# Optimization experiments

Measured on AMD Instinct MI355X. Metric: run time of the kernel, lower is better.

The kernel has to match this reference:

```python
import jax, jax.numpy as jnp
import numpy as np

NEG_SLOPE = 0.2  # LeakyReLU slope used throughout the torch module
K = 20           # hard-coded in Net.__init__ (self.k = 20)


def leaky(x):
    return jnp.where(x >= 0, x, NEG_SLOPE * x)


def setup_inputs() -> dict:
    key = jax.random.key(0)
    ks = jax.random.split(key, 11)
    B, N = 8, 2048
    Cin, Co = 6, 64  # AGConv(3*2, 64, 3*2)
    x = jax.random.normal(ks[0], (B, 3, N), dtype=jnp.float32)
    # 1x1 conv weights (bias=False in the torch code)
    W0 = jax.random.normal(ks[1], (Co, Cin), dtype=jnp.float32) / np.sqrt(Cin)      # AGConv.conv0
    W1 = jax.random.normal(ks[2], (Co * Cin, Co), dtype=jnp.float32) / np.sqrt(Co)  # AGConv.conv1
    Wc = jax.random.normal(ks[3], (3, Co), dtype=jnp.float32) / np.sqrt(Co)         # Net.conv1
    # inference-mode BatchNorm folded to per-channel scale/shift
    bn0_s = jax.random.uniform(ks[4], (Co,), minval=0.5, maxval=1.5)
    bn0_b = 0.1 * jax.random.normal(ks[5], (Co,))
    bn1_s = jax.random.uniform(ks[6], (Co,), minval=0.5, maxval=1.5)
    bn1_b = 0.1 * jax.random.normal(ks[7], (Co,))
    bnc_s = jax.random.uniform(ks[8], (3,), minval=0.5, maxval=1.5)
    bnc_b = 0.1 * jax.random.normal(ks[9], (3,))
    return dict(x=x, W0=W0, bn0_s=bn0_s, bn0_b=bn0_b, W1=W1, bn1_s=bn1_s,
                bn1_b=bn1_b, Wc=Wc, bnc_s=bnc_s, bnc_b=bnc_b)


def reference(x, W0, bn0_s, bn0_b, W1, bn1_s, bn1_b, Wc, bnc_s, bnc_b):
    B, C, N = x.shape  # [B, 3, N]
    xt = jnp.transpose(x, (0, 2, 1))  # [B, N, 3]
    inner = jnp.einsum('bci,bcj->bij', x, x)          # [B, N, N]
    xx = jnp.sum(x * x, axis=1)                       # [B, N]
    pd = 2.0 * inner - xx[:, :, None] - xx[:, None, :]
    _, idx = jax.lax.top_k(pd, K)                     # [B, N, K] int32
    # get_graph_feature: gather neighbor coords, concat (nbr - ctr, ctr)
    nbr = xt[jnp.arange(B)[:, None, None], idx]       # [B, N, K, 3]
    ctr = jnp.broadcast_to(xt[:, :, None, :], (B, N, K, C))
    e = jnp.concatenate([nbr - ctr, ctr], axis=-1)    # [B, N, K, 6]
    # p == e here since both get_graph_feature calls use the same input & idx
    # AGConv: generate per-edge [64,6] weights from e, apply to e
    y = leaky(jnp.einsum('bnki,oi->bnko', e, W0) * bn0_s + bn0_b)   # [B, N, K, 64]
    y = jnp.einsum('bnko,po->bnkp', y, W1).reshape(B, N, K, 64, 6)  # per-edge weight mats
    out = jnp.einsum('bnkoi,bnki->bnko', y, e)                      # adaptive conv
    out = leaky(out * bn1_s + bn1_b)                                # [B, N, K, 64]
    # max-pool aggregate over neighbors
    x1 = jnp.max(out, axis=2)                                       # [B, N, 64]
    # Net.conv1: 1x1 conv 64->3 + BN + leaky
    z = leaky(jnp.einsum('bno,co->bnc', x1, Wc) * bnc_s + bnc_b)    # [B, N, 3]
    return jnp.transpose(z, (0, 2, 1))                              # [B, 3, N]
```

## Files before the change

### kernel.cpp

```cpp
#include <hip/hip_runtime.h>

#define NEGSLOPE 0.2f
#define NINF (-3.4e38f)

typedef _Float16 half8 __attribute__((ext_vector_type(8)));
typedef float f32x4 __attribute__((ext_vector_type(4)));
typedef unsigned long long u64;

#define YSTRIDE 72

__device__ __forceinline__ half8 h8zero() {
    half8 z;
#pragma unroll
    for (int i = 0; i < 8; ++i) z[i] = (_Float16)0.f;
    return z;
}

__device__ __forceinline__ unsigned umin(unsigned a, unsigned b) { return a < b ? a : b; }
__device__ __forceinline__ unsigned umax(unsigned a, unsigned b) { return a > b ? a : b; }

template <int CTRL>
__device__ __forceinline__ unsigned dpp_movm(unsigned v) {
    return (unsigned)__builtin_amdgcn_update_dpp(-1, (int)v, CTRL, 0xF, 0xF, false);
}

__global__ __launch_bounds__(256) void topk_kernel(
    const float* __restrict__ x, int* __restrict__ idx_out,
    const float* __restrict__ w1, _Float16* __restrict__ w1g,
    const float* __restrict__ w0, _Float16* __restrict__ w0f,
    f32x4* __restrict__ xt) {
    if (blockIdx.x >= 4096) {
        const int pid = blockIdx.x - 4096;
        int tid = pid * 256 + threadIdx.x;
#pragma unroll
        for (int it = 0; it < 12; ++it, tid += 2048) {
            int j = tid & 7;
            int L = (tid >> 3) & 63;
            int r = tid >> 9;
            int t4 = r & 3;
            int ks = r >> 2;
            int q = L >> 4, c = L & 15;
            int i = ks >> 1;
            int o = 32 * (ks & 1) + 8 * q + j;
            int u = 16 * t4 + c;
            w1g[tid] = (_Float16)w1[(u * 6 + i) * 64 + o];
        }
        if (pid == 0) {
#pragma unroll
            for (int s = 0; s < 2; ++s) {
                int t2 = threadIdx.x * 2 + s;
                int r8 = t2 >> 3, j = t2 & 7;
                w0f[t2] = (j < 6) ? (_Float16)w0[r8 * 6 + j] : (_Float16)0.f;
            }
        }
        int base = pid * 2048;
#pragma unroll
        for (int it = 0; it < 8; ++it) {
            int i = base + it * 256 + threadIdx.x;
            int bb = i >> 11, n = i & 2047;
            const float* xbp = x + bb * 6144;
            xt[i] = (f32x4){xbp[n], xbp[2048 + n], xbp[4096 + n], 0.f};
        }
        return;
    }

    const int wave = threadIdx.x >> 6;
    const int lane = threadIdx.x & 63;
    const int row = blockIdx.x * 4 + wave;
    const int b = row >> 11;
    const int n = row & 2047;
    const float* xb = x + b * 6144;
    const float xn0 = xb[n];
    const float xn1 = xb[2048 + n];
    const float xn2 = xb[4096 + n];

    unsigned r0 = 0xFFFFFFFFu, r1 = 0xFFFFFFFFu;
    unsigned r2 = 0xFFFFFFFFu, r3 = 0xFFFFFFFFu;
    unsigned g5k = 0xFFFFFFFFu;

#pragma unroll
    for (int t = 0; t < 32; ++t) {
        const int j = t * 64 + lane;
        const float dx = xb[j] - xn0;
        const float dy = xb[2048 + j] - xn1;
        const float dz = xb[4096 + j] - xn2;
        const float d = dx * dx + dy * dy + dz * dz;
        unsigned p = (__float_as_uint(d) & 0xFFFFF800u) | (unsigned)j;
        unsigned q0 = umin(r0, p); p = umax(r0, p); r0 = q0;
        unsigned q1 = umin(r1, p); p = umax(r1, p); r1 = q1;
        unsigned q2 = umin(r2, p); p = umax(r2, p); r2 = q2;
        unsigned q3 = umin(r3, p); p = umax(r3, p); r3 = q3;
        g5k = umin(g5k, p);
    }

    if (lane & 1) {
        unsigned t0 = r0; r0 = r3; r3 = t0;
        unsigned t1 = r1; r1 = r2; r2 = t1;
    }

#define CROSS(DL, KK)                                                         \
    {                                                                         \
        const bool asc = ((lane >> ((KK) - 2)) & 1) == 0;                     \
        const bool low = (lane & (DL)) == 0;                                  \
        const bool selmin = (asc == low);                                     \
        const unsigned p0 = (unsigned)__shfl_xor((int)r0, (DL), 64);          \
        const unsigned p1 = (unsigned)__shfl_xor((int)r1, (DL), 64);          \
        const unsigned p2 = (unsigned)__shfl_xor((int)r2, (DL), 64);          \
        const unsigned p3 = (unsigned)__shfl_xor((int)r3, (DL), 64);          \
        r0 = selmin ? umin(r0, p0) : umax(r0, p0);                            \
        r1 = selmin ? umin(r1, p1) : umax(r1, p1);                            \
        r2 = selmin ? umin(r2, p2) : umax(r2, p2);                            \
        r3 = selmin ? umin(r3, p3) : umax(r3, p3);                            \
    }
#define INLANE(KK)                                                            \
    {                                                                         \
        const bool asc = ((lane >> ((KK) - 2)) & 1) == 0;                     \
        { unsigned lo = umin(r0, r2), hi = umax(r0, r2);                      \
          r0 = asc ? lo : hi; r2 = asc ? hi : lo; }                           \
        { unsigned lo = umin(r1, r3), hi = umax(r1, r3);                      \
          r1 = asc ? lo : hi; r3 = asc ? hi : lo; }                           \
        { unsigned lo = umin(r0, r1), hi = umax(r0, r1);                      \
          r0 = asc ? lo : hi; r1 = asc ? hi : lo; }                           \
        { unsigned lo = umin(r2, r3), hi = umax(r2, r3);                      \
          r2 = asc ? lo : hi; r3 = asc ? hi : lo; }                           \
    }

    CROSS(1, 3)  INLANE(3)
    CROSS(2, 4)  CROSS(1, 4)  INLANE(4)
    CROSS(4, 5)  CROSS(2, 5)  CROSS(1, 5)  INLANE(5)
    CROSS(8, 6)  CROSS(4, 6)  CROSS(2, 6)  CROSS(1, 6)  INLANE(6)
    CROSS(16, 7) CROSS(8, 7)  CROSS(4, 7)  CROSS(2, 7)  CROSS(1, 7)  INLANE(7)
    CROSS(32, 8) CROSS(16, 8) CROSS(8, 8)  CROSS(4, 8)  CROSS(2, 8)  CROSS(1, 8)
    INLANE(8)
#undef CROSS
#undef INLANE

    const int out_base = row * 20;
    const unsigned T20p = (unsigned)__builtin_amdgcn_readlane((int)r3, 4);
    const u64 bad = __ballot(g5k < T20p);

    if (bad == 0) {
        if (lane < 5) {
            int4 v;
            v.x = (int)(r0 & 2047u); v.y = (int)(r1 & 2047u);
            v.z = (int)(r2 & 2047u); v.w = (int)(r3 & 2047u);
            *(int4*)(idx_out + out_base + lane * 4) = v;
        }
    } else {
        unsigned Tprev = 0u;
#pragma unroll 1
        for (int r = 0; r < 20; ++r) {
            unsigned best = 0xFFFFFFFFu;
#pragma unroll
            for (int t = 0; t < 32; ++t) {
                const int j = t * 64 + lane;
                const float dx = xb[j] - xn0;
                const float dy = xb[2048 + j] - xn1;
                const float dz = xb[4096 + j] - xn2;
                const float d = dx * dx + dy * dy + dz * dz;
                const unsigned p = (__float_as_uint(d) & 0xFFFFF800u) | (unsigned)j;
                const bool ok = (r == 0) || (p > Tprev);
                best = umin(best, ok ? p : 0xFFFFFFFFu);
            }
            { unsigned o = dpp_movm<0x111>(best); best = umin(best, o); }
            { unsigned o = dpp_movm<0x112>(best); best = umin(best, o); }
            { unsigned o = dpp_movm<0x114>(best); best = umin(best, o); }
            { unsigned o = dpp_movm<0x118>(best); best = umin(best, o); }
            { unsigned o = dpp_movm<0x142>(best); best = umin(best, o); }
            { unsigned o = dpp_movm<0x143>(best); best = umin(best, o); }
            const unsigned K = (unsigned)__builtin_amdgcn_readlane((int)best, 63);
            if (lane == 0) idx_out[out_base + r] = (int)(K & 2047u);
            Tprev = K;
        }
    }
}

__global__ __launch_bounds__(128, 3) void mlp_mfma(
    const f32x4* __restrict__ xt, const int* __restrict__ idx,
    const _Float16* __restrict__ w0f, const float* __restrict__ bn0s,
    const float* __restrict__ bn0b, const _Float16* __restrict__ w1g,
    const float* __restrict__ bn1s, const float* __restrict__ bn1b,
    const float* __restrict__ wc, const float* __restrict__ bncs,
    const float* __restrict__ bncb, float* __restrict__ out) {
    __shared__ __align__(16) _Float16 yL[2][80 * YSTRIDE];
    __shared__ __align__(16) half8 eL[2][80];
    const int wave = threadIdx.x >> 6;
    const int lane = threadIdx.x & 63;
    const int q = lane >> 4, c = lane & 15;
    const int gw = blockIdx.x * 2 + wave;
    const int b = gw >> 9;
    const int P0 = (gw & 511) * 4;
    _Float16* yw = yL[wave];
    half8* ew = eL[wave];
    const f32x4* xtb = xt + (b << 11);

    {
        const int k = lane >> 2, pt = lane & 3;
        const int n = P0 + pt;
        const int j = idx[(b * 2048 + n) * 20 + k];
        const f32x4 cc = xtb[n];
        const f32x4 nb = xtb[j];
        half8 ev;
        ev[0] = (_Float16)(nb[0] - cc[0]); ev[1] = (_Float16)(nb[1] - cc[1]);
        ev[2] = (_Float16)(nb[2] - cc[2]); ev[3] = (_Float16)cc[0];
        ev[4] = (_Float16)cc[1];           ev[5] = (_Float16)cc[2];
        ev[6] = (_Float16)0.f;             ev[7] = (_Float16)0.f;
        ew[lane] = ev;
    }
    if (lane < 16) {
        const int el = 64 + lane;
        const int k = el >> 2, pt = el & 3;
        const int n = P0 + pt;
        const int j = idx[(b * 2048 + n) * 20 + k];
        const f32x4 cc = xtb[n];
        const f32x4 nb = xtb[j];
        half8 ev;
        ev[0] = (_Float16)(nb[0] - cc[0]); ev[1] = (_Float16)(nb[1] - cc[1]);
        ev[2] = (_Float16)(nb[2] - cc[2]); ev[3] = (_Float16)cc[0];
        ev[4] = (_Float16)cc[1];           ev[5] = (_Float16)cc[2];
        ev[6] = (_Float16)0.f;             ev[7] = (_Float16)0.f;
        ew[el] = ev;
    }

    const half8* w0f8 = (const half8*)w0f;
    const half8 z8 = h8zero();
    half8 B1[4];
    float s0v[4], b0v[4];
#pragma unroll
    for (int nt = 0; nt < 4; ++nt) {
        const half8 v = w0f8[nt * 16 + c];
        B1[nt] = (q == 0) ? v : z8;
        s0v[nt] = bn0s[16 * nt + c];
        b0v[nt] = bn0b[16 * nt + c];
    }
#pragma unroll
    for (int mt = 0; mt < 5; ++mt) {
        const half8 ev = ew[16 * mt + c];
        const half8 Ae = (q == 0) ? ev : z8;
        const int ebase = 16 * mt + 4 * q;
#pragma unroll
        for (int nt = 0; nt < 4; ++nt) {
            f32x4 D = {0.f, 0.f, 0.f, 0.f};
            D = __builtin_amdgcn_mfma_f32_16x16x32_f16(Ae, B1[nt], D, 0, 0, 0);
#pragma unroll
            for (int r = 0; r < 4; ++r) {
                float v = D[r] * s0v[nt] + b0v[nt];
                v = fmaxf(v, NEGSLOPE * v);
                const int edge = ebase + r;
                yw[edge * YSTRIDE + ((16 * nt + c) ^ (edge & 0x38))] =
                    (_Float16)v;
            }
        }
    }

    const half8* w1g8 = (const half8*)w1g;

    f32x4 acc[5][4];
#pragma unroll
    for (int mm = 0; mm < 5; ++mm)
#pragma unroll
        for (int t4 = 0; t4 < 4; ++t4) acc[mm][t4] = (f32x4){0.f, 0.f, 0.f, 0.f};

#pragma unroll 1
    for (int i6 = 0; i6 < 6; ++i6) {
        _Float16 es[5];
#pragma unroll
        for (int mm = 0; mm < 5; ++mm)
            es[mm] = ((const _Float16*)(ew + 16 * mm + c))[i6];
#pragma unroll
        for (int ks2 = 0; ks2 < 2; ++ks2) {
            const int ks = 2 * i6 + ks2;
            half8 B[4];
#pragma unroll
            for (int t4 = 0; t4 < 4; ++t4)
                B[t4] = w1g8[(ks * 4 + t4) * 64 + lane];
#pragma unroll
            for (int mm = 0; mm < 5; ++mm) {
                const int rrow = 16 * mm + c;
                const half8 Af = *(const half8*)&yw[rrow * YSTRIDE +
                                                    ((32 * ks2 + 8 * q) ^ (rrow & 0x38))];
                const half8 An = Af * es[mm];
#pragma unroll
                for (int t4 = 0; t4 < 4; ++t4)
                    acc[mm][t4] = __builtin_amdgcn_mfma_f32_16x16x32_f16(
                        An, B[t4], acc[mm][t4], 0, 0, 0);
            }
        }
    }

    float bs1[4], bb1[4];
#pragma unroll
    for (int t4 = 0; t4 < 4; ++t4) {
        bs1[t4] = bn1s[16 * t4 + c];
        bb1[t4] = bn1b[16 * t4 + c];
    }

    float x1[4][4];
#pragma unroll
    for (int r = 0; r < 4; ++r)
#pragma unroll
        for (int t4 = 0; t4 < 4; ++t4) {
            float v = NINF;
#pragma unroll
            for (int mm = 0; mm < 5; ++mm) {
                float w = acc[mm][t4][r] * bs1[t4] + bb1[t4];
                w = fmaxf(w, NEGSLOPE * w);
                v = fmaxf(v, w);
            }
            v = fmaxf(v, __shfl_xor(v, 16, 64));
            v = fmaxf(v, __shfl_xor(v, 32, 64));
            x1[r][t4] = v;
        }

    float wcv[3][4];
#pragma unroll
    for (int co = 0; co < 3; ++co)
#pragma unroll
        for (int t4 = 0; t4 < 4; ++t4) wcv[co][t4] = wc[co * 64 + 16 * t4 + c];

    float part[4][3];
#pragma unroll
    for (int r = 0; r < 4; ++r)
#pragma unroll
        for (int co = 0; co < 3; ++co) {
            float s = x1[r][0] * wcv[co][0] + x1[r][1] * wcv[co][1] +
                      x1[r][2] * wcv[co][2] + x1[r][3] * wcv[co][3];
#pragma unroll
            for (int d = 1; d < 16; d <<= 1) s += __shfl_xor(s, d, 64);
            part[r][co] = s;
        }

    if (c == 0 && q < 3) {
        const float sc = bncs[q], bc = bncb[q];
#pragma unroll
        for (int r = 0; r < 4; ++r) {
            float z = part[r][q] * sc + bc;
            z = fmaxf(z, NEGSLOPE * z);
            out[(b * 3 + q) * 2048 + P0 + r] = z;
        }
    }
}

extern "C" void kernel_launch(void* const* d_in, const int* in_sizes, int n_in,
                              void* d_out, int out_size, void* d_ws, size_t ws_size,
                              hipStream_t stream) {
    const float* x    = (const float*)d_in[0];
    const float* W0   = (const float*)d_in[1];
    const float* bn0s = (const float*)d_in[2];
    const float* bn0b = (const float*)d_in[3];
    const float* W1   = (const float*)d_in[4];
    const float* bn1s = (const float*)d_in[5];
    const float* bn1b = (const float*)d_in[6];
    const float* Wc   = (const float*)d_in[7];
    const float* bncs = (const float*)d_in[8];
    const float* bncb = (const float*)d_in[9];

    _Float16* w1g = (_Float16*)d_ws;
    _Float16* w0f = (_Float16*)((char*)d_ws + 49152);
    f32x4* xt = (f32x4*)((char*)d_ws + 65536);
    int* idx = (int*)((char*)d_ws + 327680);

    topk_kernel<<<4104, 256, 0, stream>>>(x, idx, W1, w1g, W0, w0f, xt);
    mlp_mfma<<<2048, 128, 0, stream>>>(xt, idx, w0f, bn0s, bn0b, w1g,
                                       bn1s, bn1b, Wc, bncs, bncb,
                                       (float*)d_out);
}
```

Measured before the change: 138.0 us.

## Process two query points per wave and replace bitonic merge with radix threshold search

Each wave now handles two query rows, sharing the coordinate loads for candidate points across both distance computations, and the grid is halved to match. The per-lane 4-deep insertion lists are no longer merged by a bitonic sort. Instead, a 31-step bitwise threshold search over ballot popcounts finds the 20th smallest key, and the selected entries are compacted to output with mbcnt. This removes the shuffle-heavy sorting network but adds a serial ballot loop, doubles register pressure, and writes the neighbor indices unsorted, which matches top_k only as a set.

New measurement: 175.6 us. 27.2% more time.

```diff
diff --git a/kernel.cpp b/kernel.cpp
--- a/kernel.cpp
+++ b/kernel.cpp
@@ -18,6 +18,20 @@
 
 __device__ __forceinline__ unsigned umin(unsigned a, unsigned b) { return a < b ? a : b; }
 __device__ __forceinline__ unsigned umax(unsigned a, unsigned b) { return a > b ? a : b; }
+
+__device__ __forceinline__ int lanes_below(u64 m) {
+    return __builtin_amdgcn_mbcnt_hi((unsigned)(m >> 32),
+           __builtin_amdgcn_mbcnt_lo((unsigned)m, 0u));
+}
+
+__device__ __forceinline__ void insert4(unsigned& r0, unsigned& r1, unsigned& r2,
+                                        unsigned& r3, unsigned& g5, unsigned p) {
+    unsigned q0 = umin(r0, p); p = umax(r0, p); r0 = q0;
+    unsigned q1 = umin(r1, p); p = umax(r1, p); r1 = q1;
+    unsigned q2 = umin(r2, p); p = umax(r2, p); r2 = q2;
+    unsigned q3 = umin(r3, p); p = umax(r3, p); r3 = q3;
+    g5 = umin(g5, p);
+}
 
 template <int CTRL>
 __device__ __forceinline__ unsigned dpp_movm(unsigned v) {
@@ -29,8 +43,8 @@
     const float* __restrict__ w1, _Float16* __restrict__ w1g,
     const float* __restrict__ w0, _Float16* __restrict__ w0f,
     f32x4* __restrict__ xt) {
-    if (blockIdx.x >= 4096) {
-        const int pid = blockIdx.x - 4096;
+    if (blockIdx.x >= 2048) {
+        const int pid = blockIdx.x - 2048;
         int tid = pid * 256 + threadIdx.x;
 #pragma unroll
         for (int it = 0; it < 12; ++it, tid += 2048) {
@@ -66,87 +80,49 @@
 
     const int wave = threadIdx.x >> 6;
     const int lane = threadIdx.x & 63;
-    const int row = blockIdx.x * 4 + wave;
-    const int b = row >> 11;
-    const int n = row & 2047;
+    const int pr = blockIdx.x * 4 + wave;
+    const int b = pr >> 10;
+    const int n0 = (pr & 1023) * 2;
     const float* xb = x + b * 6144;
-    const float xn0 = xb[n];
-    const float xn1 = xb[2048 + n];
-    const float xn2 = xb[4096 + n];
-
-    unsigned r0 = 0xFFFFFFFFu, r1 = 0xFFFFFFFFu;
-    unsigned r2 = 0xFFFFFFFFu, r3 = 0xFFFFFFFFu;
-    unsigned g5k = 0xFFFFFFFFu;
+    const float ax = xb[n0],     ay = xb[2048 + n0], az = xb[4096 + n0];
+    const float bx = xb[n0 + 1], by = xb[2049 + n0], bz = xb[4097 + n0];
+
+    unsigned A0 = ~0u, A1 = ~0u, A2 = ~0u, A3 = ~0u, g5A = ~0u;
+    unsigned B0 = ~0u, B1 = ~0u, B2 = ~0u, B3 = ~0u, g5B = ~0u;
 
 #pragma unroll
     for (int t = 0; t < 32; ++t) {
         const int j = t * 64 + lane;
-        const float dx = xb[j] - xn0;
-        const float dy = xb[2048 + j] - xn1;
-        const float dz = xb[4096 + j] - xn2;
-        const float d = dx * dx + dy * dy + dz * dz;
-        unsigned p = (__float_as_uint(d) & 0xFFFFF800u) | (unsigned)j;
-        unsigned q0 = umin(r0, p); p = umax(r0, p); r0 = q0;
-        unsigned q1 = umin(r1, p); p = umax(r1, p); r1 = q1;
-        unsigned q2 = umin(r2, p); p = umax(r2, p); r2 = q2;
-        unsigned q3 = umin(r3, p); p = umax(r3, p); r3 = q3;
-        g5k = umin(g5k, p);
-    }
-
-    if (lane & 1) {
-        unsigned t0 = r0; r0 = r3; r3 = t0;
-        unsigned t1 = r1; r1 = r2; r2 = t1;
-    }
-
-#define CROSS(DL, KK)                                                         \
-    {                                                                         \
-        const bool asc = ((lane >> ((KK) - 2)) & 1) == 0;                     \
-        const bool low = (lane & (DL)) == 0;                                  \
-        const bool selmin = (asc == low);                                     \
-        const unsigned p0 = (unsigned)__shfl_xor((int)r0, (DL), 64);          \
-        const unsigned p1 = (unsigned)__shfl_xor((int)r1, (DL), 64);          \
-        const unsigned p2 = (unsigned)__shfl_xor((int)r2, (DL), 64);          \
-        const unsigned p3 = (unsigned)__shfl_xor((int)r3, (DL), 64);          \
-        r0 = selmin ? umin(r0, p0) : umax(r0, p0);                            \
-        r1 = selmin ? umin(r1, p1) : umax(r1, p1);                            \
-        r2 = selmin ? umin(r2, p2) : umax(r2, p2);                            \
-        r3 = selmin ? umin(r3, p3) : umax(r3, p3);                            \
-    }
-#define INLANE(KK)                                                            \
-    {                                                                         \
-        const bool asc = ((lane >> ((KK) - 2)) & 1) == 0;                     \
-        { unsigned lo = umin(r0, r2), hi = umax(r0, r2);                      \
-          r0 = asc ? lo : hi; r2 = asc ? hi : lo; }                           \
-        { unsigned lo = umin(r1, r3), hi = umax(r1, r3);                      \
-          r1 = asc ? lo : hi; r3 = asc ? hi : lo; }                           \
-        { unsigned lo = umin(r0, r1), hi = umax(r0, r1);                      \
-          r0 = asc ? lo : hi; r1 = asc ? hi : lo; }                           \
-        { unsigned lo = umin(r2, r3), hi = umax(r2, r3);                      \
-          r2 = asc ? lo : hi; r3 = asc ? hi : lo; }                           \
-    }
-
-    CROSS(1, 3)  INLANE(3)
-    CROSS(2, 4)  CROSS(1, 4)  INLANE(4)
-    CROSS(4, 5)  CROSS(2, 5)  CROSS(1, 5)  INLANE(5)
-    CROSS(8, 6)  CROSS(4, 6)  CROSS(2, 6)  CROSS(1, 6)  INLANE(6)
-    CROSS(16, 7) CROSS(8, 7)  CROSS(4, 7)  CROSS(2, 7)  CROSS(1, 7)  INLANE(7)
-    CROSS(32, 8) CROSS(16, 8) CROSS(8, 8)  CROSS(4, 8)  CROSS(2, 8)  CROSS(1, 8)
-    INLANE(8)
-#undef CROSS
-#undef INLANE
-
-    const int out_base = row * 20;
-    const unsigned T20p = (unsigned)__builtin_amdgcn_readlane((int)r3, 4);
-    const u64 bad = __ballot(g5k < T20p);
-
-    if (bad == 0) {
-        if (lane < 5) {
-            int4 v;
-            v.x = (int)(r0 & 2047u); v.y = (int)(r1 & 2047u);
-            v.z = (int)(r2 & 2047u); v.w = (int)(r3 & 2047u);
-            *(int4*)(idx_out + out_base + lane * 4) = v;
-        }
-    } else {
+        const float x0 = xb[j], x1 = xb[2048 + j], x2 = xb[4096 + j];
+        const float dxa = x0 - ax, dya = x1 - ay, dza = x2 - az;
+        const float dxb = x0 - bx, dyb = x1 - by, dzb = x2 - bz;
+        const float dA = dxa * dxa + dya * dya + dza * dza;
+        const float dB = dxb * dxb + dyb * dyb + dzb * dzb;
+        const unsigned pA = (__float_as_uint(dA) & 0xFFFFF800u) | (unsigned)j;
+        const unsigned pB = (__float_as_uint(dB) & 0xFFFFF800u) | (unsigned)j;
+        insert4(A0, A1, A2, A3, g5A, pA);
+        insert4(B0, B1, B2, B3, g5B, pB);
+    }
+
+    unsigned TA = 0u, TB = 0u;
+#pragma unroll 1
+    for (int bit = 30; bit >= 0; --bit) {
+        const unsigned cA = TA | (1u << bit);
+        const unsigned cB = TB | (1u << bit);
+        const int ca = __popcll(__ballot(A0 < cA)) + __popcll(__ballot(A1 < cA)) +
+                       __popcll(__ballot(A2 < cA)) + __popcll(__ballot(A3 < cA));
+        const int cb = __popcll(__ballot(B0 < cB)) + __popcll(__ballot(B1 < cB)) +
+                       __popcll(__ballot(B2 < cB)) + __popcll(__ballot(B3 < cB));
+        if (ca <= 19) TA = cA;
+        if (cb <= 19) TB = cB;
+    }
+
+    const int obA = (b * 2048 + n0) * 20;
+    const int obB = obA + 20;
+    const u64 badA = __ballot(g5A < TA);
+    const u64 badB = __ballot(g5B < TB);
+
+    auto fallback = [&](float cx, float cy, float cz, int ob) {
         unsigned Tprev = 0u;
 #pragma unroll 1
         for (int r = 0; r < 20; ++r) {
@@ -154,9 +130,9 @@
 #pragma unroll
             for (int t = 0; t < 32; ++t) {
                 const int j = t * 64 + lane;
-                const float dx = xb[j] - xn0;
-                const float dy = xb[2048 + j] - xn1;
-                const float dz = xb[4096 + j] - xn2;
+                const float dx = xb[j] - cx;
+                const float dy = xb[2048 + j] - cy;
+                const float dz = xb[4096 + j] - cz;
                 const float d = dx * dx + dy * dy + dz * dz;
                 const unsigned p = (__float_as_uint(d) & 0xFFFFF800u) | (unsigned)j;
                 const bool ok = (r == 0) || (p > Tprev);
@@ -169,9 +145,37 @@
             { unsigned o = dpp_movm<0x142>(best); best = umin(best, o); }
             { unsigned o = dpp_movm<0x143>(best); best = umin(best, o); }
             const unsigned K = (unsigned)__builtin_amdgcn_readlane((int)best, 63);
-            if (lane == 0) idx_out[out_base + r] = (int)(K & 2047u);
+            if (lane == 0) idx_out[ob + r] = (int)(K & 2047u);
             Tprev = K;
         }
+    };
+
+    if (badA == 0) {
+        const u64 m0 = __ballot(A0 <= TA), m1 = __ballot(A1 <= TA);
+        const u64 m2 = __ballot(A2 <= TA), m3 = __ballot(A3 <= TA);
+        const int s1 = __popcll(m0);
+        const int s2 = s1 + __popcll(m1);
+        const int s3 = s2 + __popcll(m2);
+        if (A0 <= TA) idx_out[obA + lanes_below(m0)] = (int)(A0 & 2047u);
+        if (A1 <= TA) idx_out[obA + s1 + lanes_below(m1)] = (int)(A1 & 2047u);
+        if (A2 <= TA) idx_out[obA + s2 + lanes_below(m2)] = (int)(A2 & 2047u);
+        if (A3 <= TA) idx_out[obA + s3 + lanes_below(m3)] = (int)(A3 & 2047u);
+    } else {
+        fallback(ax, ay, az, obA);
+    }
+
+    if (badB == 0) {
+        const u64 m0 = __ballot(B0 <= TB), m1 = __ballot(B1 <= TB);
+        const u64 m2 = __ballot(B2 <= TB), m3 = __ballot(B3 <= TB);
+        const int s1 = __popcll(m0);
+        const int s2 = s1 + __popcll(m1);
+        const int s3 = s2 + __popcll(m2);
+        if (B0 <= TB) idx_out[obB + lanes_below(m0)] = (int)(B0 & 2047u);
+        if (B1 <= TB) idx_out[obB + s1 + lanes_below(m1)] = (int)(B1 & 2047u);
+        if (B2 <= TB) idx_out[obB + s2 + lanes_below(m2)] = (int)(B2 & 2047u);
+        if (B3 <= TB) idx_out[obB + s3 + lanes_below(m3)] = (int)(B3 & 2047u);
+    } else {
+        fallback(bx, by, bz, obB);
     }
 }
 
@@ -360,7 +364,7 @@
     f32x4* xt = (f32x4*)((char*)d_ws + 65536);
     int* idx = (int*)((char*)d_ws + 327680);
 
-    topk_kernel<<<4104, 256, 0, stream>>>(x, idx, W1, w1g, W0, w0f, xt);
+    topk_kernel<<<2056, 256, 0, stream>>>(x, idx, W1, w1g, W0, w0f, xt);
     mlp_mfma<<<2048, 128, 0, stream>>>(xt, idx, w0f, bn0s, bn0b, w1g,
                                        bn1s, bn1b, Wc, bncs, bncb,
                                        (float*)d_out);
```
